# Kernel optimization log

Measured on AMD Instinct MI355X. Metric: run time of the kernel, lower is better.

Reference implementation:

```python
import jax, jax.numpy as jnp
import numpy as np

B, T, F, H = 1024, 512, 16, 64


def setup_inputs() -> dict:
    key = jax.random.key(0)
    ks = jax.random.split(key, 8)
    return {
        "x": jax.random.normal(ks[0], (B, T, F), jnp.float32),
        "W": jax.random.normal(ks[1], (F, 3 * H), jnp.float32) * 0.1,
        "U": jax.random.normal(ks[2], (H, 3 * H), jnp.float32) * 0.1,
        "b": jax.random.normal(ks[3], (2, 3 * H), jnp.float32) * 0.1,
        "w1": jax.random.normal(ks[4], (H, 64), jnp.float32) * 0.1,
        "b1": jax.random.normal(ks[5], (64,), jnp.float32) * 0.1,
        "gamma": jnp.ones((64,), jnp.float32),
        "beta": jnp.zeros((64,), jnp.float32),
        "mov_mean": jnp.zeros((64,), jnp.float32),
        "mov_var": jnp.ones((64,), jnp.float32),
        "w2": jax.random.normal(ks[6], (64, 1), jnp.float32) * 0.1,
        "b2": jax.random.normal(ks[7], (1,), jnp.float32) * 0.1,
    }


def _gru_last(x, W, U, b):
    # Keras GRU, reset_after=True, inference (no dropout). Returns last hidden state [B,H].
    b_i, b_r = b[0], b[1]
    xp = jnp.einsum("btf,fg->btg", x, W) + b_i  # [B,T,3H] precomputed input projections
    xp_t = jnp.transpose(xp, (1, 0, 2))          # [T,B,3H]
    h0 = jnp.zeros((x.shape[0], H), x.dtype)

    def step(h, xpt):
        rec = h @ U + b_r                         # [B,3H]
        xz, xr, xh = jnp.split(xpt, 3, axis=-1)
        rz, rr, rh = jnp.split(rec, 3, axis=-1)
        z = jax.nn.sigmoid(xz + rz)
        r = jax.nn.sigmoid(xr + rr)
        hh = jnp.tanh(xh + r * rh)
        h_new = z * h + (1.0 - z) * hh
        return h_new, None

    h_last, _ = jax.lax.scan(step, h0, xp_t)
    return h_last


def reference(x, W, U, b, w1, b1, gamma, beta, mov_mean, mov_var, w2, b2):
    h = _gru_last(x, W, U, b)                     # [B,H]
    y = jax.nn.relu(h @ w1 + b1)                  # Dense(64, relu)
    # Dropout: identity in inference. BatchNorm: inference with moving stats.
    eps = 1e-3  # Keras BatchNormalization default epsilon
    y = (y - mov_mean) * jax.lax.rsqrt(mov_var + eps) * gamma + beta
    out = y @ w2 + b2                             # [B,1]
    return out
```

## Files before the change

### kernel.cpp

```cpp
#include <hip/hip_runtime.h>
#include <hip/hip_fp16.h>


#define T_ 512
#define F_ 16
#define H_ 64
#define ROWS_ 16
#define HSS 80

typedef _Float16 half_t;
typedef _Float16 h8 __attribute__((ext_vector_type(8)));
typedef float f32x4 __attribute__((ext_vector_type(4)));

__device__ __forceinline__ float fast_rcp(float a) {
    return __builtin_amdgcn_rcpf(a);
}
__device__ __forceinline__ float sigm(float a) {
    return fast_rcp(1.0f + __expf(-a));
}
__device__ __forceinline__ float tanh_fast(float a) {
    return 1.0f - 2.0f * fast_rcp(__expf(2.0f * a) + 1.0f);
}

__global__ __launch_bounds__(256, 1) void gru_fused(
    const float* __restrict__ x, const float* __restrict__ W,
    const float* __restrict__ U, const float* __restrict__ b,
    const float* __restrict__ w1, const float* __restrict__ b1,
    const float* __restrict__ gamma_, const float* __restrict__ beta_,
    const float* __restrict__ mmean, const float* __restrict__ mvar,
    const float* __restrict__ w2, const float* __restrict__ b2,
    float* __restrict__ out)
{
    __shared__ __align__(16) half_t hs[2][ROWS_][HSS];
    __shared__ float hf[ROWS_][H_ + 4];

    const int tid = threadIdx.x;
    const int w   = tid >> 6;
    const int l   = tid & 63;
    const int c   = l & 15;
    const int q   = l >> 4;
    const int r0  = blockIdx.x * ROWS_;
    const int col = 16 * w + c;

    for (int i = tid; i < 2 * ROWS_ * HSS; i += 256)
        ((half_t*)hs)[i] = (half_t)0.0f;

    h8 buz[2], bur[2], buh[2];
    #pragma unroll
    for (int cc = 0; cc < 2; ++cc) {
        #pragma unroll
        for (int i = 0; i < 8; ++i) {
            const int k = 32 * cc + 8 * q + i;
            buz[cc][i] = (half_t)U[k * 192 +       col];
            bur[cc][i] = (half_t)U[k * 192 +  64 + col];
            buh[cc][i] = (half_t)U[k * 192 + 128 + col];
        }
    }
    h8 bwz, bwr, bwh;
    #pragma unroll
    for (int i = 0; i < 8; ++i) {
        const int k = 8 * q + i;
        const bool real = (q < 2);
        bwz[i] = real ? (half_t)W[k * 192 +       col] : (half_t)0.0f;
        bwr[i] = real ? (half_t)W[k * 192 +  64 + col] : (half_t)0.0f;
        bwh[i] = real ? (half_t)W[k * 192 + 128 + col] : (half_t)0.0f;
    }
    const float bz  = b[col]       + b[192 + col];
    const float br_ = b[64 + col]  + b[256 + col];
    const float bxh = b[128 + col];
    const float brh = b[320 + col];

    __syncthreads();

    float hold[4] = {0.f, 0.f, 0.f, 0.f};

    const float* xrow = x + (size_t)(r0 + c) * (T_ * F_) + 8 * (q & 1);
    float4 xfa = *(const float4*)(xrow);
    float4 xfb = *(const float4*)(xrow + 4);

    for (int t = 0; t < T_; ++t) {
        const int nb = t & 1;

        h8 ax;
        ax[0] = (half_t)xfa.x; ax[1] = (half_t)xfa.y;
        ax[2] = (half_t)xfa.z; ax[3] = (half_t)xfa.w;
        ax[4] = (half_t)xfb.x; ax[5] = (half_t)xfb.y;
        ax[6] = (half_t)xfb.z; ax[7] = (half_t)xfb.w;

        const int tn = (t + 1 < T_) ? (t + 1) : t;
        const float4 nxa = *(const float4*)(xrow + tn * F_);
        const float4 nxb = *(const float4*)(xrow + tn * F_ + 4);

        const half_t* hrow = &hs[nb][c][0];
        const h8 ah0 = *(const h8*)(hrow + 8 * q);
        const h8 ah1 = *(const h8*)(hrow + 32 + 8 * q);

        f32x4 cz  = {bz,  bz,  bz,  bz };
        f32x4 cr  = {br_, br_, br_, br_};
        f32x4 crh = {brh, brh, brh, brh};
        f32x4 cxh = {bxh, bxh, bxh, bxh};
        cz  = __builtin_amdgcn_mfma_f32_16x16x32_f16(ax,  bwz,    cz,  0, 0, 0);
        cr  = __builtin_amdgcn_mfma_f32_16x16x32_f16(ax,  bwr,    cr,  0, 0, 0);
        cxh = __builtin_amdgcn_mfma_f32_16x16x32_f16(ax,  bwh,    cxh, 0, 0, 0);
        cz  = __builtin_amdgcn_mfma_f32_16x16x32_f16(ah0, buz[0], cz,  0, 0, 0);
        cr  = __builtin_amdgcn_mfma_f32_16x16x32_f16(ah0, bur[0], cr,  0, 0, 0);
        crh = __builtin_amdgcn_mfma_f32_16x16x32_f16(ah0, buh[0], crh, 0, 0, 0);
        cz  = __builtin_amdgcn_mfma_f32_16x16x32_f16(ah1, buz[1], cz,  0, 0, 0);
        cr  = __builtin_amdgcn_mfma_f32_16x16x32_f16(ah1, bur[1], cr,  0, 0, 0);
        crh = __builtin_amdgcn_mfma_f32_16x16x32_f16(ah1, buh[1], crh, 0, 0, 0);

        half_t* wrp = &hs[nb ^ 1][0][0] + col;
        #pragma unroll
        for (int i = 0; i < 4; ++i) {
            const float z  = sigm(cz[i]);
            const float r  = sigm(cr[i]);
            const float hh = tanh_fast(fmaf(r, crh[i], cxh[i]));
            hold[i] = fmaf(z, hold[i] - hh, hh);
            wrp[(4 * q + i) * HSS] = (half_t)hold[i];
        }

        xfa = nxa; xfb = nxb;
        __syncthreads();
    }

    #pragma unroll
    for (int i = 0; i < 4; ++i)
        hf[4 * q + i][col] = hold[i];
    __syncthreads();

    const int j = l;
    float y0 = b1[j], y1 = y0, y2 = y0, y3 = y0;
    #pragma unroll 8
    for (int k = 0; k < H_; ++k) {
        const float wk = w1[k * 64 + j];
        y0 = fmaf(hf[4 * w + 0][k], wk, y0);
        y1 = fmaf(hf[4 * w + 1][k], wk, y1);
        y2 = fmaf(hf[4 * w + 2][k], wk, y2);
        y3 = fmaf(hf[4 * w + 3][k], wk, y3);
    }
    const float sc = rsqrtf(mvar[j] + 1e-3f) * gamma_[j];
    const float mm = mmean[j], bt = beta_[j], v2 = w2[j];
    float yy[4] = {y0, y1, y2, y3};
    #pragma unroll
    for (int ri = 0; ri < 4; ++ri) {
        float yv = fmaxf(yy[ri], 0.0f);
        yv = (yv - mm) * sc + bt;
        float acc = yv * v2;
        #pragma unroll
        for (int off = 32; off > 0; off >>= 1)
            acc += __shfl_down(acc, off, 64);
        if (l == 0) out[r0 + 4 * w + ri] = acc + b2[0];
    }
}

extern "C" void kernel_launch(void* const* d_in, const int* in_sizes, int n_in,
                              void* d_out, int out_size, void* d_ws, size_t ws_size,
                              hipStream_t stream) {
    const float* x      = (const float*)d_in[0];
    const float* W      = (const float*)d_in[1];
    const float* U      = (const float*)d_in[2];
    const float* b      = (const float*)d_in[3];
    const float* w1     = (const float*)d_in[4];
    const float* b1     = (const float*)d_in[5];
    const float* gamma_ = (const float*)d_in[6];
    const float* beta_  = (const float*)d_in[7];
    const float* mmean  = (const float*)d_in[8];
    const float* mvar   = (const float*)d_in[9];
    const float* w2     = (const float*)d_in[10];
    const float* b2     = (const float*)d_in[11];
    float* out = (float*)d_out;

    const int B = in_sizes[0] / (T_ * F_);
    gru_fused<<<B / ROWS_, 256, 0, stream>>>(x, W, U, b, w1, b1, gamma_, beta_,
                                             mmean, mvar, w2, b2, out);
}
```

Before: 304.8 us.

## Split GRU gates across two wave groups with shared-memory handoff

Doubles the block to 512 threads. Waves 0-3 compute the z and r gates with MFMA plus sigmoid and publish them to shared memory. Waves 4-7 compute the candidate-state MFMAs, then combine and update h. Input biases are folded into the MFMA by setting one activation lane to 1 and placing the bias in the weight fragment. The goal is to shorten the per-step serial critical path by running the gate work on more waves, at the cost of an extra barrier per timestep and fp16-rounded biases.

```diff
diff --git a/kernel.cpp b/kernel.cpp
--- a/kernel.cpp
+++ b/kernel.cpp
@@ -22,7 +22,7 @@
     return 1.0f - 2.0f * fast_rcp(__expf(2.0f * a) + 1.0f);
 }
 
-__global__ __launch_bounds__(256, 1) void gru_fused(
+__global__ __launch_bounds__(512, 1) void gru_fused(
     const float* __restrict__ x, const float* __restrict__ W,
     const float* __restrict__ U, const float* __restrict__ b,
     const float* __restrict__ w1, const float* __restrict__ b1,
@@ -32,43 +32,53 @@
     float* __restrict__ out)
 {
     __shared__ __align__(16) half_t hs[2][ROWS_][HSS];
+    __shared__ __align__(16) float  zrz[4][64][4];
+    __shared__ __align__(16) float  zrr[4][64][4];
     __shared__ float hf[ROWS_][H_ + 4];
 
     const int tid = threadIdx.x;
-    const int w   = tid >> 6;
+    const int wid = tid >> 6;
+    const bool isH = (wid >= 4);
+    const int g   = wid & 3;
     const int l   = tid & 63;
     const int c   = l & 15;
     const int q   = l >> 4;
     const int r0  = blockIdx.x * ROWS_;
-    const int col = 16 * w + c;
-
-    for (int i = tid; i < 2 * ROWS_ * HSS; i += 256)
+    const int col = 16 * g + c;
+
+    for (int i = tid; i < 2 * ROWS_ * HSS; i += 512)
         ((half_t*)hs)[i] = (half_t)0.0f;
 
-    h8 buz[2], bur[2], buh[2];
-    #pragma unroll
-    for (int cc = 0; cc < 2; ++cc) {
-        #pragma unroll
-        for (int i = 0; i < 8; ++i) {
-            const int k = 32 * cc + 8 * q + i;
-            buz[cc][i] = (half_t)U[k * 192 +       col];
-            bur[cc][i] = (half_t)U[k * 192 +  64 + col];
-            buh[cc][i] = (half_t)U[k * 192 + 128 + col];
-        }
-    }
-    h8 bwz, bwr, bwh;
-    #pragma unroll
-    for (int i = 0; i < 8; ++i) {
-        const int k = 8 * q + i;
-        const bool real = (q < 2);
-        bwz[i] = real ? (half_t)W[k * 192 +       col] : (half_t)0.0f;
-        bwr[i] = real ? (half_t)W[k * 192 +  64 + col] : (half_t)0.0f;
-        bwh[i] = real ? (half_t)W[k * 192 + 128 + col] : (half_t)0.0f;
-    }
     const float bz  = b[col]       + b[192 + col];
     const float br_ = b[64 + col]  + b[256 + col];
     const float bxh = b[128 + col];
     const float brh = b[320 + col];
+
+    h8 bu_p0, bu_p1, bu_q0, bu_q1, bw_p, bw_q;
+    if (!isH) {
+        #pragma unroll
+        for (int i = 0; i < 8; ++i) {
+            const int k = 8 * q + i;
+            bu_p0[i] = (half_t)U[k * 192 + col];
+            bu_p1[i] = (half_t)U[(32 + k) * 192 + col];
+            bu_q0[i] = (half_t)U[k * 192 + 64 + col];
+            bu_q1[i] = (half_t)U[(32 + k) * 192 + 64 + col];
+            bw_p[i] = (q < 2) ? (half_t)W[k * 192 + col]
+                              : ((q == 2 && i == 0) ? (half_t)bz  : (half_t)0.0f);
+            bw_q[i] = (q < 2) ? (half_t)W[k * 192 + 64 + col]
+                              : ((q == 2 && i == 0) ? (half_t)br_ : (half_t)0.0f);
+        }
+    } else {
+        #pragma unroll
+        for (int i = 0; i < 8; ++i) {
+            const int k = 8 * q + i;
+            bu_p0[i] = (half_t)U[k * 192 + 128 + col];
+            bu_p1[i] = (half_t)U[(32 + k) * 192 + 128 + col];
+            bw_p[i] = (q < 2) ? (half_t)W[k * 192 + 128 + col]
+                              : ((q == 2 && i == 0) ? (half_t)bxh : (half_t)0.0f);
+            bu_q0[i] = (half_t)0.0f; bu_q1[i] = (half_t)0.0f; bw_q[i] = (half_t)0.0f;
+        }
+    }
 
     __syncthreads();
 
@@ -86,6 +96,7 @@
         ax[2] = (half_t)xfa.z; ax[3] = (half_t)xfa.w;
         ax[4] = (half_t)xfb.x; ax[5] = (half_t)xfb.y;
         ax[6] = (half_t)xfb.z; ax[7] = (half_t)xfb.w;
+        if (q == 2) ax[0] = (half_t)1.0f;
 
         const int tn = (t + 1 < T_) ? (t + 1) : t;
         const float4 nxa = *(const float4*)(xrow + tn * F_);
@@ -95,61 +106,82 @@
         const h8 ah0 = *(const h8*)(hrow + 8 * q);
         const h8 ah1 = *(const h8*)(hrow + 32 + 8 * q);
 
-        f32x4 cz  = {bz,  bz,  bz,  bz };
-        f32x4 cr  = {br_, br_, br_, br_};
-        f32x4 crh = {brh, brh, brh, brh};
-        f32x4 cxh = {bxh, bxh, bxh, bxh};
-        cz  = __builtin_amdgcn_mfma_f32_16x16x32_f16(ax,  bwz,    cz,  0, 0, 0);
-        cr  = __builtin_amdgcn_mfma_f32_16x16x32_f16(ax,  bwr,    cr,  0, 0, 0);
-        cxh = __builtin_amdgcn_mfma_f32_16x16x32_f16(ax,  bwh,    cxh, 0, 0, 0);
-        cz  = __builtin_amdgcn_mfma_f32_16x16x32_f16(ah0, buz[0], cz,  0, 0, 0);
-        cr  = __builtin_amdgcn_mfma_f32_16x16x32_f16(ah0, bur[0], cr,  0, 0, 0);
-        crh = __builtin_amdgcn_mfma_f32_16x16x32_f16(ah0, buh[0], crh, 0, 0, 0);
-        cz  = __builtin_amdgcn_mfma_f32_16x16x32_f16(ah1, buz[1], cz,  0, 0, 0);
-        cr  = __builtin_amdgcn_mfma_f32_16x16x32_f16(ah1, bur[1], cr,  0, 0, 0);
-        crh = __builtin_amdgcn_mfma_f32_16x16x32_f16(ah1, buh[1], crh, 0, 0, 0);
-
-        half_t* wrp = &hs[nb ^ 1][0][0] + col;
-        #pragma unroll
-        for (int i = 0; i < 4; ++i) {
-            const float z  = sigm(cz[i]);
-            const float r  = sigm(cr[i]);
-            const float hh = tanh_fast(fmaf(r, crh[i], cxh[i]));
-            hold[i] = fmaf(z, hold[i] - hh, hh);
-            wrp[(4 * q + i) * HSS] = (half_t)hold[i];
-        }
+        if (!isH) {
+            f32x4 cp = {0.f, 0.f, 0.f, 0.f};
+            f32x4 cq = {0.f, 0.f, 0.f, 0.f};
+            cp = __builtin_amdgcn_mfma_f32_16x16x32_f16(ax,  bw_p,  cp, 0, 0, 0);
+            cq = __builtin_amdgcn_mfma_f32_16x16x32_f16(ax,  bw_q,  cq, 0, 0, 0);
+            cp = __builtin_amdgcn_mfma_f32_16x16x32_f16(ah0, bu_p0, cp, 0, 0, 0);
+            cq = __builtin_amdgcn_mfma_f32_16x16x32_f16(ah0, bu_q0, cq, 0, 0, 0);
+            cp = __builtin_amdgcn_mfma_f32_16x16x32_f16(ah1, bu_p1, cp, 0, 0, 0);
+            cq = __builtin_amdgcn_mfma_f32_16x16x32_f16(ah1, bu_q1, cq, 0, 0, 0);
+            *(float4*)&zrz[g][l][0] =
+                make_float4(sigm(cp[0]), sigm(cp[1]), sigm(cp[2]), sigm(cp[3]));
+            *(float4*)&zrr[g][l][0] =
+                make_float4(sigm(cq[0]), sigm(cq[1]), sigm(cq[2]), sigm(cq[3]));
+        } else {
+            f32x4 crh = {brh, brh, brh, brh};
+            f32x4 cxh = {0.f, 0.f, 0.f, 0.f};
+            cxh = __builtin_amdgcn_mfma_f32_16x16x32_f16(ax,  bw_p,  cxh, 0, 0, 0);
+            crh = __builtin_amdgcn_mfma_f32_16x16x32_f16(ah0, bu_p0, crh, 0, 0, 0);
+            crh = __builtin_amdgcn_mfma_f32_16x16x32_f16(ah1, bu_p1, crh, 0, 0, 0);
+
+            __syncthreads();
+
+            const float4 zv = *(const float4*)&zrz[g][l][0];
+            const float4 rv = *(const float4*)&zrr[g][l][0];
+            half_t* wrp = &hs[nb ^ 1][0][0] + col;
+            {
+                const float hh0 = tanh_fast(fmaf(rv.x, crh[0], cxh[0]));
+                const float hh1 = tanh_fast(fmaf(rv.y, crh[1], cxh[1]));
+                const float hh2 = tanh_fast(fmaf(rv.z, crh[2], cxh[2]));
+                const float hh3 = tanh_fast(fmaf(rv.w, crh[3], cxh[3]));
+                hold[0] = fmaf(zv.x, hold[0] - hh0, hh0);
+                hold[1] = fmaf(zv.y, hold[1] - hh1, hh1);
+                hold[2] = fmaf(zv.z, hold[2] - hh2, hh2);
+                hold[3] = fmaf(zv.w, hold[3] - hh3, hh3);
+                wrp[(4 * q + 0) * HSS] = (half_t)hold[0];
+                wrp[(4 * q + 1) * HSS] = (half_t)hold[1];
+                wrp[(4 * q + 2) * HSS] = (half_t)hold[2];
+                wrp[(4 * q + 3) * HSS] = (half_t)hold[3];
+            }
+        }
+        if (!isH) __syncthreads();
 
         xfa = nxa; xfb = nxb;
         __syncthreads();
     }
 
-    #pragma unroll
-    for (int i = 0; i < 4; ++i)
-        hf[4 * q + i][col] = hold[i];
+    if (isH) {
+        #pragma unroll
+        for (int i = 0; i < 4; ++i)
+            hf[4 * q + i][col] = hold[i];
+    }
     __syncthreads();
-
-    const int j = l;
-    float y0 = b1[j], y1 = y0, y2 = y0, y3 = y0;
-    #pragma unroll 8
-    for (int k = 0; k < H_; ++k) {
-        const float wk = w1[k * 64 + j];
-        y0 = fmaf(hf[4 * w + 0][k], wk, y0);
-        y1 = fmaf(hf[4 * w + 1][k], wk, y1);
-        y2 = fmaf(hf[4 * w + 2][k], wk, y2);
-        y3 = fmaf(hf[4 * w + 3][k], wk, y3);
-    }
-    const float sc = rsqrtf(mvar[j] + 1e-3f) * gamma_[j];
-    const float mm = mmean[j], bt = beta_[j], v2 = w2[j];
-    float yy[4] = {y0, y1, y2, y3};
-    #pragma unroll
-    for (int ri = 0; ri < 4; ++ri) {
-        float yv = fmaxf(yy[ri], 0.0f);
-        yv = (yv - mm) * sc + bt;
-        float acc = yv * v2;
-        #pragma unroll
-        for (int off = 32; off > 0; off >>= 1)
-            acc += __shfl_down(acc, off, 64);
-        if (l == 0) out[r0 + 4 * w + ri] = acc + b2[0];
+    if (!isH) {
+        const int j = l;
+        float y0 = b1[j], y1 = y0, y2 = y0, y3 = y0;
+        #pragma unroll 8
+        for (int k = 0; k < H_; ++k) {
+            const float wk = w1[k * 64 + j];
+            y0 = fmaf(hf[4 * g + 0][k], wk, y0);
+            y1 = fmaf(hf[4 * g + 1][k], wk, y1);
+            y2 = fmaf(hf[4 * g + 2][k], wk, y2);
+            y3 = fmaf(hf[4 * g + 3][k], wk, y3);
+        }
+        const float sc = rsqrtf(mvar[j] + 1e-3f) * gamma_[j];
+        const float mm = mmean[j], bt = beta_[j], v2 = w2[j];
+        float yy[4] = {y0, y1, y2, y3};
+        #pragma unroll
+        for (int ri = 0; ri < 4; ++ri) {
+            float yv = fmaxf(yy[ri], 0.0f);
+            yv = (yv - mm) * sc + bt;
+            float acc = yv * v2;
+            #pragma unroll
+            for (int off = 32; off > 0; off >>= 1)
+                acc += __shfl_down(acc, off, 64);
+            if (l == 0) out[r0 + 4 * g + ri] = acc + b2[0];
+        }
     }
 }
 
@@ -171,6 +203,6 @@
     float* out = (float*)d_out;
 
     const int B = in_sizes[0] / (T_ * F_);
-    gru_fused<<<B / ROWS_, 256, 0, stream>>>(x, W, U, b, w1, b1, gamma_, beta_,
+    gru_fused<<<B / ROWS_, 512, 0, stream>>>(x, W, U, b, w1, b1, gamma_, beta_,
                                              mmean, mvar, w2, b2, out);
 }
```

Measured after the change: 347.4 us. +14.0%, slower.
